# Kernel tuning notes

Measured on AMD Instinct MI355X. Metric: run time of the kernel, lower is better.

Reference implementation:

```python
import jax, jax.numpy as jnp
import numpy as np
import math

IN_F = 512
OUT_F = 512
N_EXPERTS = 8
N_GROUPS = 32
TOKENS_PER_GROUP = 2048
N_TOKENS = N_GROUPS * TOKENS_PER_GROUP


def setup_inputs() -> dict:
    key = jax.random.key(0)
    ks = jax.random.split(key, 6)
    k = math.sqrt(1.0 / IN_F)  # init scale from reset_parameters
    x = jax.random.normal(ks[0], (N_TOKENS, IN_F), dtype=jnp.float32)
    # routing coefficients per group (e.g. softmax-like positive weights)
    coefficients = jax.random.uniform(ks[1], (N_GROUPS, N_EXPERTS), dtype=jnp.float32)
    coefficients = coefficients / coefficients.sum(axis=1, keepdims=True)
    weight_experts = jax.random.uniform(ks[2], (N_EXPERTS, OUT_F, IN_F), minval=-k, maxval=k, dtype=jnp.float32)
    bias_experts = jax.random.uniform(ks[3], (N_EXPERTS, OUT_F), minval=-k, maxval=k, dtype=jnp.float32)
    weight_shared = jax.random.uniform(ks[4], (OUT_F, IN_F), minval=-k, maxval=k, dtype=jnp.float32)
    bias_shared = jax.random.uniform(ks[5], (OUT_F,), minval=-k, maxval=k, dtype=jnp.float32)
    sizes = jnp.full((N_GROUPS,), TOKENS_PER_GROUP, dtype=jnp.int32)
    return {
        "x": x,
        "coefficients": coefficients,
        "weight_experts": weight_experts,
        "bias_experts": bias_experts,
        "weight_shared": weight_shared,
        "bias_shared": bias_shared,
        "sizes": sizes,
    }


def reference(x, coefficients, weight_experts, bias_experts, weight_shared, bias_shared, sizes):
    # Routed path: per-group mixed weights  W_g = sum_e coeff[g,e] * W_e  (+ shared)
    G = coefficients.shape[0]
    N = x.shape[0]
    T = N // G  # equal group sizes (static), equivalent to torch.split(x, sizes)
    mixed_w = jnp.einsum('ge,eoi->goi', coefficients, weight_experts) + weight_shared[None]
    mixed_b = jnp.einsum('ge,eo->go', coefficients, bias_experts) + bias_shared[None]
    xg = x.reshape(G, T, -1)                      # [G, T, in]
    out = jnp.einsum('gti,goi->gto', xg, mixed_w) # grouped GEMM, F.linear per group
    out = out + mixed_b[:, None, :]
    return out.reshape(N, -1)
```

## Files before the change

### kernel.cpp

```cpp
#include <hip/hip_runtime.h>
#include <stdint.h>

typedef unsigned short u16;
typedef __attribute__((ext_vector_type(8))) __bf16 bf16x8;
typedef __attribute__((ext_vector_type(4))) float f32x4;

#define NGROUPS 32
#define TOK 2048
#define IN_F 512
#define OUT_F 512
#define NEXP 8
#define BM 128
#define BN 128
#define BK 64

__device__ __forceinline__ u16 f2bf(float f) {
    unsigned int u = __float_as_uint(f);
    unsigned int r = (u + 0x7fffu + ((u >> 16) & 1u)) >> 16;
    return (u16)r;
}

__global__ __launch_bounds__(256) void mix_w_kernel(
    const float* __restrict__ coeff, const float* __restrict__ We,
    const float* __restrict__ Wsh, u16* __restrict__ mw)
{
    __shared__ float cs[NGROUPS * NEXP];
    int tid = threadIdx.x;
    cs[tid] = coeff[tid];
    __syncthreads();

    size_t idx = ((size_t)blockIdx.x * 256 + tid) * 4;
    f32x4 wsh = *(const f32x4*)(Wsh + idx);
    f32x4 we[NEXP];
#pragma unroll
    for (int e = 0; e < NEXP; ++e)
        we[e] = *(const f32x4*)(We + (size_t)e * OUT_F * IN_F + idx);

    for (int g = 0; g < NGROUPS; ++g) {
        f32x4 a = wsh;
#pragma unroll
        for (int e = 0; e < NEXP; ++e) {
            float c = cs[g * NEXP + e];
            a[0] += c * we[e][0];
            a[1] += c * we[e][1];
            a[2] += c * we[e][2];
            a[3] += c * we[e][3];
        }
        unsigned int ow[2];
        ow[0] = (unsigned int)f2bf(a[0]) | ((unsigned int)f2bf(a[1]) << 16);
        ow[1] = (unsigned int)f2bf(a[2]) | ((unsigned int)f2bf(a[3]) << 16);
        *(uint2*)(mw + (size_t)g * OUT_F * IN_F + idx) = *(const uint2*)ow;
    }
}

__global__ __launch_bounds__(256) void gemm_kernel(
    const float* __restrict__ x, const u16* __restrict__ mw,
    const float* __restrict__ coeff, const float* __restrict__ be,
    const float* __restrict__ bsh, float* __restrict__ out)
{
    __shared__ __align__(16) float As[BM * BK];
    __shared__ __align__(16) u16  Bs[BN * BK];

    int bid = blockIdx.x;
    int g = bid >> 6;
    int t = bid & 63;
    int mtile = t >> 2;
    int ntile = t & 3;

    const float* Ag = x + ((size_t)g * TOK + (size_t)mtile * BM) * IN_F;
    const u16*   Bg = mw + (size_t)g * OUT_F * IN_F + (size_t)ntile * BN * IN_F;

    int tid  = threadIdx.x;
    int lane = tid & 63;
    int wave = tid >> 6;
    int wm = wave >> 1, wn = wave & 1;
    int lm = lane & 15, lq = lane >> 4;

    int srA = tid >> 4;
    int scA = (tid & 15) * 4;
    int srB = tid >> 3;
    int scB = (tid & 7) * 8;

    f32x4 acc[4][4];
#pragma unroll
    for (int mi = 0; mi < 4; ++mi)
#pragma unroll
        for (int ni = 0; ni < 4; ++ni)
            acc[mi][ni] = f32x4{0.f, 0.f, 0.f, 0.f};

    for (int k0 = 0; k0 < IN_F; k0 += BK) {
        __syncthreads();
#pragma unroll
        for (int p = 0; p < 8; ++p) {
            int r = srA + p * 16;
            __builtin_amdgcn_global_load_lds(
                (const __attribute__((address_space(1))) void*)(Ag + (size_t)r * IN_F + k0 + scA),
                (__attribute__((address_space(3))) void*)(As + r * BK + scA),
                16, 0, 0);
        }
#pragma unroll
        for (int p = 0; p < 4; ++p) {
            int r = srB + p * 32;
            __builtin_amdgcn_global_load_lds(
                (const __attribute__((address_space(1))) void*)(Bg + (size_t)r * IN_F + k0 + scB),
                (__attribute__((address_space(3))) void*)(Bs + r * BK + scB),
                16, 0, 0);
        }
        __syncthreads();

#pragma unroll
        for (int ks = 0; ks < 2; ++ks) {
            bf16x8 af[4], bfv[4];
#pragma unroll
            for (int mi = 0; mi < 4; ++mi) {
                int base = (wm * 64 + mi * 16 + lm) * BK + ks * 32 + lq * 8;
                f32x4 a0 = *(const f32x4*)&As[base];
                f32x4 a1 = *(const f32x4*)&As[base + 4];
#pragma unroll
                for (int j = 0; j < 4; ++j) {
                    af[mi][j]     = (__bf16)a0[j];
                    af[mi][j + 4] = (__bf16)a1[j];
                }
            }
#pragma unroll
            for (int ni = 0; ni < 4; ++ni)
                bfv[ni] = *(const bf16x8*)&Bs[(wn * 64 + ni * 16 + lm) * BK + ks * 32 + lq * 8];
#pragma unroll
            for (int mi = 0; mi < 4; ++mi)
#pragma unroll
                for (int ni = 0; ni < 4; ++ni)
                    acc[mi][ni] = __builtin_amdgcn_mfma_f32_16x16x32_bf16(
                        af[mi], bfv[ni], acc[mi][ni], 0, 0, 0);
        }
    }

    int c0 = ntile * BN + wn * 64;
    float cg[NEXP];
#pragma unroll
    for (int e = 0; e < NEXP; ++e) cg[e] = coeff[g * NEXP + e];
    float bias[4];
#pragma unroll
    for (int ni = 0; ni < 4; ++ni) {
        int o = c0 + ni * 16 + lm;
        float v = bsh[o];
#pragma unroll
        for (int e = 0; e < NEXP; ++e) v += cg[e] * be[e * OUT_F + o];
        bias[ni] = v;
    }

    size_t rowbase = (size_t)g * TOK + (size_t)mtile * BM + (size_t)wm * 64;
#pragma unroll
    for (int mi = 0; mi < 4; ++mi) {
#pragma unroll
        for (int rr = 0; rr < 4; ++rr) {
            size_t row = rowbase + mi * 16 + lq * 4 + rr;
            float* orow = out + row * OUT_F;
#pragma unroll
            for (int ni = 0; ni < 4; ++ni)
                orow[c0 + ni * 16 + lm] = acc[mi][ni][rr] + bias[ni];
        }
    }
}

extern "C" void kernel_launch(void* const* d_in, const int* in_sizes, int n_in,
                              void* d_out, int out_size, void* d_ws, size_t ws_size,
                              hipStream_t stream) {
    const float* x     = (const float*)d_in[0];
    const float* coeff = (const float*)d_in[1];
    const float* We    = (const float*)d_in[2];
    const float* be    = (const float*)d_in[3];
    const float* Wsh   = (const float*)d_in[4];
    const float* bsh   = (const float*)d_in[5];
    float* out = (float*)d_out;

    u16* mw = (u16*)d_ws;

    mix_w_kernel<<<OUT_F * IN_F / (256 * 4), 256, 0, stream>>>(coeff, We, Wsh, mw);

    int grid = NGROUPS * (TOK / BM) * (OUT_F / BN);
    gemm_kernel<<<grid, 256, 0, stream>>>(x, mw, coeff, be, bsh, out);
}
```

Measured before the change: 306.1 us.

## Stage A as bf16 via registers with XOR-swizzled LDS, XCD-aware group mapping

The GEMM now loads x tiles into registers as fp32, converts them to bf16 once, and stores them into a half-size, XOR-swizzled LDS tile. The next k-tile's A loads are prefetched into registers while MFMAs run on the current one. The B tile is also swizzled via global_load_lds addressing to avoid LDS bank conflicts. Blocks are remapped so each XCD handles whole groups for L2 locality, and the weight-mixing kernel is split across 4 grid rows for more parallelism. Register pressure grows because of the prefetch buffer.

Result: faster. 293.4 us (-4.2%).

```diff
diff --git a/kernel.cpp b/kernel.cpp
--- a/kernel.cpp
+++ b/kernel.cpp
@@ -3,6 +3,7 @@
 
 typedef unsigned short u16;
 typedef __attribute__((ext_vector_type(8))) __bf16 bf16x8;
+typedef __attribute__((ext_vector_type(4))) __bf16 bf16x4;
 typedef __attribute__((ext_vector_type(4))) float f32x4;
 
 #define NGROUPS 32
@@ -36,7 +37,8 @@
     for (int e = 0; e < NEXP; ++e)
         we[e] = *(const f32x4*)(We + (size_t)e * OUT_F * IN_F + idx);
 
-    for (int g = 0; g < NGROUPS; ++g) {
+    int g0 = blockIdx.y * 8;
+    for (int g = g0; g < g0 + 8; ++g) {
         f32x4 a = wsh;
 #pragma unroll
         for (int e = 0; e < NEXP; ++e) {
@@ -58,12 +60,14 @@
     const float* __restrict__ coeff, const float* __restrict__ be,
     const float* __restrict__ bsh, float* __restrict__ out)
 {
-    __shared__ __align__(16) float As[BM * BK];
-    __shared__ __align__(16) u16  Bs[BN * BK];
+    __shared__ __align__(16) u16 As[BM * BK];
+    __shared__ __align__(16) u16 Bs[BN * BK];
 
     int bid = blockIdx.x;
-    int g = bid >> 6;
-    int t = bid & 63;
+    int xcd = bid & 7;
+    int i   = bid >> 3;
+    int g = xcd * 4 + (i >> 6);
+    int t = i & 63;
     int mtile = t >> 2;
     int ntile = t & 3;
 
@@ -76,11 +80,6 @@
     int wm = wave >> 1, wn = wave & 1;
     int lm = lane & 15, lq = lane >> 4;
 
-    int srA = tid >> 4;
-    int scA = (tid & 15) * 4;
-    int srB = tid >> 3;
-    int scB = (tid & 7) * 8;
-
     f32x4 acc[4][4];
 #pragma unroll
     for (int mi = 0; mi < 4; ++mi)
@@ -88,43 +87,63 @@
         for (int ni = 0; ni < 4; ++ni)
             acc[mi][ni] = f32x4{0.f, 0.f, 0.f, 0.f};
 
-    for (int k0 = 0; k0 < IN_F; k0 += BK) {
+    f32x4 areg[8];
+#pragma unroll
+    for (int j = 0; j < 8; ++j) {
+        int L = j * 256 + tid;
+        areg[j] = *(const f32x4*)(Ag + (size_t)(L >> 4) * IN_F + (L & 15) * 4);
+    }
+
+    for (int kk = 0; kk < IN_F / BK; ++kk) {
+        int k0 = kk * BK;
         __syncthreads();
-#pragma unroll
-        for (int p = 0; p < 8; ++p) {
-            int r = srA + p * 16;
+
+#pragma unroll
+        for (int j = 0; j < 8; ++j) {
+            int L = j * 256 + tid;
+            int r = L >> 4, c4 = L & 15;
+            int p = (c4 >> 1) ^ (r & 7);
+            bf16x4 bv;
+            bv[0] = (__bf16)areg[j][0];
+            bv[1] = (__bf16)areg[j][1];
+            bv[2] = (__bf16)areg[j][2];
+            bv[3] = (__bf16)areg[j][3];
+            *(bf16x4*)(As + r * 64 + p * 8 + (c4 & 1) * 4) = bv;
+        }
+#pragma unroll
+        for (int q = 0; q < 4; ++q) {
+            int r = q * 32 + (tid >> 3);
+            int c = (tid & 7) ^ (r & 7);
             __builtin_amdgcn_global_load_lds(
-                (const __attribute__((address_space(1))) void*)(Ag + (size_t)r * IN_F + k0 + scA),
-                (__attribute__((address_space(3))) void*)(As + r * BK + scA),
+                (const __attribute__((address_space(1))) void*)(Bg + (size_t)r * IN_F + k0 + c * 8),
+                (__attribute__((address_space(3))) void*)(Bs + ((size_t)q * 256 + tid) * 8),
                 16, 0, 0);
         }
-#pragma unroll
-        for (int p = 0; p < 4; ++p) {
-            int r = srB + p * 32;
-            __builtin_amdgcn_global_load_lds(
-                (const __attribute__((address_space(1))) void*)(Bg + (size_t)r * IN_F + k0 + scB),
-                (__attribute__((address_space(3))) void*)(Bs + r * BK + scB),
-                16, 0, 0);
-        }
         __syncthreads();
+
+        if (kk + 1 < IN_F / BK) {
+#pragma unroll
+            for (int j = 0; j < 8; ++j) {
+                int L = j * 256 + tid;
+                areg[j] = *(const f32x4*)(Ag + (size_t)(L >> 4) * IN_F + (k0 + BK) + (L & 15) * 4);
+            }
+        }
 
 #pragma unroll
         for (int ks = 0; ks < 2; ++ks) {
             bf16x8 af[4], bfv[4];
 #pragma unroll
             for (int mi = 0; mi < 4; ++mi) {
-                int base = (wm * 64 + mi * 16 + lm) * BK + ks * 32 + lq * 8;
-                f32x4 a0 = *(const f32x4*)&As[base];
-                f32x4 a1 = *(const f32x4*)&As[base + 4];
-#pragma unroll
-                for (int j = 0; j < 4; ++j) {
-                    af[mi][j]     = (__bf16)a0[j];
-                    af[mi][j + 4] = (__bf16)a1[j];
-                }
+                int r = wm * 64 + mi * 16 + lm;
+                int p = (ks * 4 + lq) ^ (r & 7);
+                af[mi] = *(const bf16x8*)(As + r * 64 + p * 8);
             }
 #pragma unroll
-            for (int ni = 0; ni < 4; ++ni)
-                bfv[ni] = *(const bf16x8*)&Bs[(wn * 64 + ni * 16 + lm) * BK + ks * 32 + lq * 8];
+            for (int ni = 0; ni < 4; ++ni) {
+                int r = wn * 64 + ni * 16 + lm;
+                int p = (ks * 4 + lq) ^ (r & 7);
+                bfv[ni] = *(const bf16x8*)(Bs + r * 64 + p * 8);
+            }
 #pragma unroll
             for (int mi = 0; mi < 4; ++mi)
 #pragma unroll
@@ -175,7 +194,7 @@
 
     u16* mw = (u16*)d_ws;
 
-    mix_w_kernel<<<OUT_F * IN_F / (256 * 4), 256, 0, stream>>>(coeff, We, Wsh, mw);
+    mix_w_kernel<<<dim3(OUT_F * IN_F / (256 * 4), 4), 256, 0, stream>>>(coeff, We, Wsh, mw);
 
     int grid = NGROUPS * (TOK / BM) * (OUT_F / BN);
     gemm_kernel<<<grid, 256, 0, stream>>>(x, mw, coeff, be, bsh, out);
```
